# Kernel tuning notes

Hardware: AMD Instinct MI355X
Metric: run time of the kernel (lower is better)

Reference implementation:

```python
import jax, jax.numpy as jnp
import numpy as np

# Static sensor configuration (from init_kwargs)
WIDTH = 1024
HEIGHT = 1024
X0, Y0 = -1.0, -1.0
DX = (1.0 - (-1.0)) / WIDTH
DY = (1.0 - (-1.0)) / HEIGHT
SIGMA = 0.1
KERNEL_SIZE = 2

_off = np.arange(-KERNEL_SIZE, KERNEL_SIZE + 1)
_ox, _oy = np.meshgrid(_off, _off, indexing='xy')
OFF_X = jnp.asarray(_ox.flatten(), dtype=jnp.int32)  # [(2k+1)^2] = [25]
OFF_Y = jnp.asarray(_oy.flatten(), dtype=jnp.int32)

N_POINTS = 2_000_000


def setup_inputs() -> dict:
    key = jax.random.key(0)
    k1, k2, k3 = jax.random.split(key, 3)
    x = jax.random.uniform(k1, (N_POINTS,), dtype=jnp.float32)       # in [0,1) subset of bounds
    y = jax.random.uniform(k2, (N_POINTS,), dtype=jnp.float32)
    values = jax.random.normal(k3, (N_POINTS,), dtype=jnp.float32)
    return {"x": x, "y": y, "values": values}


def reference(x, y, values):
    # Map to pixel coordinates
    x_pix = (x - X0) / DX
    y_pix = (y - Y0) / DY
    xi_base = jnp.floor(x_pix).astype(jnp.int32)
    yi_base = jnp.floor(y_pix).astype(jnp.int32)
    x_frac = x_pix - xi_base
    y_frac = y_pix - yi_base

    # [N, 25] neighbor pixel indices and Gaussian weights
    xi = xi_base[:, None] + OFF_X[None, :]
    yi = yi_base[:, None] + OFF_Y[None, :]
    dist_x = x_frac[:, None] - OFF_X[None, :].astype(x_frac.dtype)
    dist_y = y_frac[:, None] - OFF_Y[None, :].astype(y_frac.dtype)
    weights = jnp.exp(-0.5 * (dist_x ** 2 + dist_y ** 2) / (SIGMA ** 2))
    weights = weights / jnp.sum(weights, axis=1, keepdims=True)

    valid = (xi >= 0) & (xi < WIDTH) & (yi >= 0) & (yi < HEIGHT)
    xi = jnp.clip(xi, 0, WIDTH - 1)
    yi = jnp.clip(yi, 0, HEIGHT - 1)

    splatted = values[:, None] * weights * valid  # [N, 25]
    flat_idx = (yi * WIDTH + xi).reshape(-1)      # [N*25]
    img_flat = jax.ops.segment_sum(splatted.reshape(-1), flat_idx,
                                   num_segments=HEIGHT * WIDTH)
    return img_flat.reshape(HEIGHT, WIDTH)
```

## Files before the change

kernel.cpp:

```cpp
#include <hip/hip_runtime.h>
#include <hip/hip_bf16.h>

#define WIDTH 1024
#define HEIGHT 1024
#define IMG_ELEMS (WIDTH * HEIGHT)
#define TPX 32
#define NTILES (TPX * TPX)
#define NB 256
#define BT 1024
#define BSTRIDE 8192
#define CAPP 36
#define PTS_CAP 8448

#define OFF_PTS   0
#define OFF_BIDX  (OFF_PTS + 2 * PTS_CAP)
#define OFF_HCNT  (OFF_BIDX + (NTILES * CAPP) / 2)
#define OFF_RCNT  (OFF_HCNT + NTILES)
#define OFF_RDST  (OFF_RCNT + NB)
#define OFF_ROFF  (OFF_RDST + NB)
#define OFF_STMP  (OFF_ROFF + NB)
#define SMEM_U32  (OFF_STMP + NB)


__device__ __forceinline__ void point_geom(float px, float py, int& cxb, int& cyb,
                                           float& ax, float& ay) {
    float xp = (px + 1.0f) * 512.0f;
    float yp = (py + 1.0f) * 512.0f;
    int xb = (int)floorf(xp);
    int yb = (int)floorf(yp);
    float xf = xp - (float)xb;
    float yf = yp - (float)yb;
    ax = 1.0f / (1.0f + __expf(100.0f * xf - 50.0f));
    ay = 1.0f / (1.0f + __expf(100.0f * yf - 50.0f));
    cxb = min(max(xb, 0), WIDTH - 1);
    cyb = min(max(yb, 0), HEIGHT - 1);
}

__global__ void __launch_bounds__(BT)
k_sortlocal(const float* __restrict__ x, const float* __restrict__ y,
            const float* __restrict__ v, uint2* __restrict__ payload,
            unsigned* __restrict__ runCnt, float4* __restrict__ outv,
            int n, int ppb) {
    __shared__ unsigned cursor[NTILES];
    __shared__ unsigned wtot[BT / 64];
    __shared__ __align__(16) uint2 stage[BSTRIDE];

    int b = blockIdx.x;
    int p = threadIdx.x;
    cursor[p] = 0u;
    outv[(unsigned)b * 1024u + p] = make_float4(0.f, 0.f, 0.f, 0.f);
    __syncthreads();

    int lo = b * ppb;
    int hi = min(n, lo + ppb);

    uint2 pay[8];
    unsigned meta[8];

    auto enc = [&](int s, float px, float py, float pv) {
        int cxb, cyb; float ax, ay;
        point_geom(px, py, cxb, cyb, ax, ay);
        unsigned tile = (unsigned)((cyb >> 5) * TPX + (cxb >> 5));
        unsigned pos = atomicAdd(&cursor[tile], 1u);
        unsigned axq = (unsigned)(ax * 2047.0f + 0.5f);
        unsigned ayq = (unsigned)(ay * 2047.0f + 0.5f);
        pay[s] = make_uint2(__float_as_uint(pv),
                            axq | (ayq << 11) | ((unsigned)(cxb & 31) << 22) |
                            ((unsigned)(cyb & 31) << 27));
        meta[s] = (tile << 16) | pos;
    };

#pragma unroll
    for (int it = 0; it < 2; ++it) {
        int base = lo + p * 4 + it * (BT * 4);
        if (base + 3 < hi) {
            float4 x4 = *(const float4*)&x[base];
            float4 y4 = *(const float4*)&y[base];
            float4 v4 = *(const float4*)&v[base];
            enc(it * 4 + 0, x4.x, y4.x, v4.x);
            enc(it * 4 + 1, x4.y, y4.y, v4.y);
            enc(it * 4 + 2, x4.z, y4.z, v4.z);
            enc(it * 4 + 3, x4.w, y4.w, v4.w);
        } else {
#pragma unroll
            for (int j = 0; j < 4; ++j) {
                int idx = base + j;
                if (idx < hi) enc(it * 4 + j, x[idx], y[idx], v[idx]);
                else          meta[it * 4 + j] = 0xFFFFFFFFu;
            }
        }
    }
    __syncthreads();

    unsigned c = cursor[p];
    unsigned lane = p & 63, w = p >> 6;
    unsigned vsc = c;
#pragma unroll
    for (int d = 1; d < 64; d <<= 1) {
        unsigned t_ = __shfl_up(vsc, d, 64);
        if (lane >= (unsigned)d) vsc += t_;
    }
    if (lane == 63) wtot[w] = vsc;
    __syncthreads();
    if (p == 0) {
        unsigned a = 0;
#pragma unroll
        for (int k = 0; k < BT / 64; ++k) { unsigned t_ = wtot[k]; wtot[k] = a; a += t_; }
    }
    __syncthreads();
    unsigned excl = vsc - c + wtot[w];
    runCnt[(unsigned)p * NB + (unsigned)b] = (excl << 16) | c;
    cursor[p] = excl;
    __syncthreads();

#pragma unroll
    for (int s = 0; s < 8; ++s) {
        unsigned m = meta[s];
        if (m != 0xFFFFFFFFu)
            stage[cursor[m >> 16] + (m & 0xFFFFu)] = pay[s];
    }
    __syncthreads();

    int nv = ppb >> 1;
    uint4* dstv = (uint4*)(payload + ((size_t)b << 13));
    const uint4* srcv = (const uint4*)stage;
    for (int i = p; i < nv; i += BT) dstv[i] = srcv[i];
}

__global__ void __launch_bounds__(BT)
k_accum(const uint2* __restrict__ payload, const unsigned* __restrict__ runCnt,
        float* __restrict__ out) {
    __shared__ unsigned smem[SMEM_U32];
    uint2*          pts  = (uint2*)&smem[OFF_PTS];
    unsigned short* bidx = (unsigned short*)&smem[OFF_BIDX];
    unsigned*       hcnt = &smem[OFF_HCNT];
    unsigned*       rcnt = &smem[OFF_RCNT];
    unsigned*       rdst = &smem[OFF_RDST];
    unsigned*       roff = &smem[OFF_ROFF];
    unsigned*       stmp = &smem[OFF_STMP];
    float*          exT01 = (float*)&smem[OFF_PTS];
    float*          exT11 = (float*)&smem[OFF_PTS + BT];

    unsigned b = blockIdx.x;
    unsigned t;
    if (b < 256u) {
        t = (16u + (b >> 4)) * 32u + 16u + (b & 15u);
    } else {
        unsigned r = b - 256u;
        if (r < 512u) t = r;
        else { unsigned q = r - 512u; t = (16u + (q >> 4)) * 32u + (q & 15u); }
    }

    int p = threadIdx.x;
    unsigned lane = p & 63, w = p >> 6;
    unsigned c0 = 0u;
    if (p < NB) {
        unsigned pk = runCnt[t * NB + (unsigned)p];
        c0 = pk & 0xFFFFu;
        rcnt[p] = c0;
        roff[p] = pk >> 16;
    }
    hcnt[p] = 0u;
    unsigned tsum = c0;
#pragma unroll
    for (int d = 32; d >= 1; d >>= 1) tsum += __shfl_down(tsum, d, 64);
    if (p < NB && lane == 0) rdst[w] = tsum;
    __syncthreads();
    unsigned total = rdst[0] + rdst[1] + rdst[2] + rdst[3];
    if (total == 0) return;

    unsigned vsc = c0;
#pragma unroll
    for (int d = 1; d < 64; d <<= 1) {
        unsigned tmp = __shfl_up(vsc, d, 64);
        if (lane >= (unsigned)d) vsc += tmp;
    }
    __syncthreads();
    if (p < NB && lane == 63) stmp[w] = vsc;
    __syncthreads();
    if (p == 0) {
        unsigned a = 0;
#pragma unroll
        for (int k = 0; k < 4; ++k) { unsigned tt = stmp[k]; stmp[k] = a; a += tt; }
    }
    __syncthreads();
    if (p < NB) rdst[p] = vsc - c0 + stmp[w];
    __syncthreads();

    unsigned sub = lane >> 3, jl = lane & 7u;
#pragma unroll
    for (int kk = 0; kk < 2; ++kk) {
        int r = (int)w * 16 + kk * 8 + (int)sub;
        unsigned cnt = rcnt[r], dst = rdst[r];
        const unsigned long long* g =
            (const unsigned long long*)(payload + (((size_t)r) << 13) + roff[r]);
        for (unsigned j = jl; j < cnt; j += 8) {
            unsigned long long raw = __builtin_nontemporal_load(&g[j]);
            uint2 pl = make_uint2((unsigned)raw, (unsigned)(raw >> 32));
            unsigned slot = dst + j;
            if (slot < PTS_CAP) {
                pts[slot] = pl;
                unsigned pix = (pl.y >> 22) & 1023u;
                unsigned pos = atomicAdd(&hcnt[pix], 1u);
                if (pos < CAPP) bidx[pix * CAPP + pos] = (unsigned short)slot;
            }
        }
    }
    __syncthreads();

    float t00 = 0.0f, t10 = 0.0f, t01 = 0.0f, t11 = 0.0f;
    unsigned cnt = min(hcnt[p], (unsigned)CAPP);
    for (unsigned e = 0; e < cnt; ++e) {
        uint2 sp = pts[bidx[p * CAPP + e]];
        float val = __uint_as_float(sp.x);
        float ax = (float)(sp.y & 2047u) * (1.0f / 2047.0f);
        float ay = (float)((sp.y >> 11) & 2047u) * (1.0f / 2047.0f);
        float bx = 1.0f - ax, by = 1.0f - ay;
        t00 += val * ax * ay;
        t10 += val * bx * ay;
        t01 += val * ax * by;
        t11 += val * bx * by;
    }
    __syncthreads();
    exT01[p] = t01;
    exT11[p] = t11;
    __syncthreads();

    int lx = p & 31, ly = p >> 5;
    int gx = (int)((t & 31u) << 5) + lx;
    int gy = (int)((t >> 5) << 5) + ly;
    size_t g = (size_t)gy * WIDTH + gx;
    float t10l = __shfl_up(t10, 1, 64);
    float sum = t00;
    if (lx > 0) sum += t10l;
    if (ly > 0) sum += exT01[p - 32];
    if (lx > 0 && ly > 0) sum += exT11[p - 33];
    if (lx == 0 || ly == 0) atomicAdd(&out[g], sum);
    else out[g] = sum;

    bool xr = (gx + 1 < WIDTH), yd = (gy + 1 < HEIGHT);
    if (lx == 31 && xr) {
        atomicAdd(&out[g + 1], t10);
        if (yd) atomicAdd(&out[g + WIDTH + 1], t11);
    }
    if (ly == 31 && yd) {
        atomicAdd(&out[g + WIDTH], t01);
        if (lx < 31 && xr) atomicAdd(&out[g + WIDTH + 1], t11);
    }
}

__global__ void __launch_bounds__(256)
splat_direct(const float* __restrict__ x, const float* __restrict__ y,
             const float* __restrict__ v, float* __restrict__ out, int n) {
    int i = blockIdx.x * blockDim.x + threadIdx.x;
    if (i >= n) return;
    int cxb, cyb; float ax, ay;
    point_geom(x[i], y[i], cxb, cyb, ax, ay);
    float val = v[i];
    float bx = 1.0f - ax, by = 1.0f - ay;
    float* row = out + cyb * WIDTH;
    atomicAdd(row + cxb, val * ax * ay);
    if (cxb + 1 < WIDTH) atomicAdd(row + cxb + 1, val * bx * ay);
    if (cyb + 1 < HEIGHT) {
        row += WIDTH;
        atomicAdd(row + cxb, val * ax * by);
        if (cxb + 1 < WIDTH) atomicAdd(row + cxb + 1, val * bx * by);
    }
}

extern "C" void kernel_launch(void* const* d_in, const int* in_sizes, int n_in,
                              void* d_out, int out_size, void* d_ws, size_t ws_size,
                              hipStream_t stream) {
    const float* x = (const float*)d_in[0];
    const float* y = (const float*)d_in[1];
    const float* v = (const float*)d_in[2];
    float* out = (float*)d_out;
    int n = in_sizes[0];
    int ppb = ((n + NB - 1) / NB + 7) & ~7;

    size_t off_payload = 0;
    size_t off_runcnt  = off_payload + (size_t)NB * BSTRIDE * sizeof(uint2);
    size_t need        = off_runcnt + (size_t)NB * NTILES * sizeof(unsigned);
    bool caps_ok = (ppb <= BSTRIDE) && (out_size == IMG_ELEMS);

    if (ws_size >= need && caps_ok) {
        char* ws = (char*)d_ws;
        uint2*    payload = (uint2*)(ws + off_payload);
        unsigned* runCnt  = (unsigned*)(ws + off_runcnt);

        k_sortlocal<<<NB, BT, 0, stream>>>(x, y, v, payload, runCnt,
                                           (float4*)out, n, ppb);
        k_accum<<<NTILES, BT, 0, stream>>>(payload, runCnt, out);
    } else {
        (void)hipMemsetAsync(out, 0, (size_t)out_size * sizeof(float), stream);
        splat_direct<<<(n + 255) / 256, 256, 0, stream>>>(x, y, v, out, n);
    }
}
```

Before: 94.49 us.

## Fuse sort and accumulate kernels into one cooperative kernel with grid sync

Result: slower. 226.7 us (+139.9%).

```diff
diff --git a/kernel.cpp b/kernel.cpp
--- a/kernel.cpp
+++ b/kernel.cpp
@@ -1,5 +1,5 @@
 #include <hip/hip_runtime.h>
-#include <hip/hip_bf16.h>
+#include <hip/hip_cooperative_groups.h>
 
 #define WIDTH 1024
 #define HEIGHT 1024
@@ -37,6 +37,219 @@
 }
 
 __global__ void __launch_bounds__(BT)
+k_fused(const float* __restrict__ x, const float* __restrict__ y,
+        const float* __restrict__ v, uint2* __restrict__ payload,
+        unsigned* __restrict__ runCnt, float* __restrict__ out,
+        int n, int ppb) {
+    __shared__ __align__(16) unsigned smem[SMEM_U32];
+    int b = blockIdx.x;
+    int p = threadIdx.x;
+    unsigned lane = p & 63, w = p >> 6;
+
+    {
+        uint2*    stage  = (uint2*)&smem[0];
+        unsigned* cursor = &smem[16384];
+        unsigned* wtot   = &smem[17408];
+
+        cursor[p] = 0u;
+        ((float4*)out)[(unsigned)b * 1024u + p] = make_float4(0.f, 0.f, 0.f, 0.f);
+        __syncthreads();
+
+        int lo = b * ppb;
+        int hi = min(n, lo + ppb);
+
+        uint2 pay[8];
+        unsigned meta[8];
+
+        auto enc = [&](int s, float px, float py, float pv) {
+            int cxb, cyb; float ax, ay;
+            point_geom(px, py, cxb, cyb, ax, ay);
+            unsigned tile = (unsigned)((cyb >> 5) * TPX + (cxb >> 5));
+            unsigned pos = atomicAdd(&cursor[tile], 1u);
+            unsigned axq = (unsigned)(ax * 2047.0f + 0.5f);
+            unsigned ayq = (unsigned)(ay * 2047.0f + 0.5f);
+            pay[s] = make_uint2(__float_as_uint(pv),
+                                axq | (ayq << 11) | ((unsigned)(cxb & 31) << 22) |
+                                ((unsigned)(cyb & 31) << 27));
+            meta[s] = (tile << 16) | pos;
+        };
+
+#pragma unroll
+        for (int it = 0; it < 2; ++it) {
+            int base = lo + p * 4 + it * (BT * 4);
+            if (base + 3 < hi) {
+                float4 x4 = *(const float4*)&x[base];
+                float4 y4 = *(const float4*)&y[base];
+                float4 v4 = *(const float4*)&v[base];
+                enc(it * 4 + 0, x4.x, y4.x, v4.x);
+                enc(it * 4 + 1, x4.y, y4.y, v4.y);
+                enc(it * 4 + 2, x4.z, y4.z, v4.z);
+                enc(it * 4 + 3, x4.w, y4.w, v4.w);
+            } else {
+#pragma unroll
+                for (int j = 0; j < 4; ++j) {
+                    int idx = base + j;
+                    if (idx < hi) enc(it * 4 + j, x[idx], y[idx], v[idx]);
+                    else          meta[it * 4 + j] = 0xFFFFFFFFu;
+                }
+            }
+        }
+        __syncthreads();
+
+        unsigned c = cursor[p];
+        unsigned vsc = c;
+#pragma unroll
+        for (int d = 1; d < 64; d <<= 1) {
+            unsigned t_ = __shfl_up(vsc, d, 64);
+            if (lane >= (unsigned)d) vsc += t_;
+        }
+        if (lane == 63) wtot[w] = vsc;
+        __syncthreads();
+        if (p == 0) {
+            unsigned a = 0;
+#pragma unroll
+            for (int k = 0; k < BT / 64; ++k) { unsigned t_ = wtot[k]; wtot[k] = a; a += t_; }
+        }
+        __syncthreads();
+        unsigned excl = vsc - c + wtot[w];
+        runCnt[(unsigned)p * NB + (unsigned)b] = (excl << 16) | c;
+        cursor[p] = excl;
+        __syncthreads();
+
+#pragma unroll
+        for (int s = 0; s < 8; ++s) {
+            unsigned m = meta[s];
+            if (m != 0xFFFFFFFFu)
+                stage[cursor[m >> 16] + (m & 0xFFFFu)] = pay[s];
+        }
+        __syncthreads();
+
+        int nv = ppb >> 1;
+        uint4* dstv = (uint4*)(payload + ((size_t)b << 13));
+        const uint4* srcv = (const uint4*)stage;
+        for (int i = p; i < nv; i += BT) dstv[i] = srcv[i];
+    }
+
+    __threadfence();
+    cooperative_groups::this_grid().sync();
+
+    uint2*          pts  = (uint2*)&smem[OFF_PTS];
+    unsigned short* bidx = (unsigned short*)&smem[OFF_BIDX];
+    unsigned*       hcnt = &smem[OFF_HCNT];
+    unsigned*       rcnt = &smem[OFF_RCNT];
+    unsigned*       rdst = &smem[OFF_RDST];
+    unsigned*       roff = &smem[OFF_ROFF];
+    unsigned*       stmp = &smem[OFF_STMP];
+    float*          exT01 = (float*)&smem[OFF_PTS];
+    float*          exT11 = (float*)&smem[OFF_PTS + BT];
+
+    for (int sub = 0; sub < 4; ++sub) {
+        unsigned bb = (unsigned)b + ((unsigned)sub << 8);
+        unsigned t;
+        if (bb < 256u) {
+            t = (16u + (bb >> 4)) * 32u + 16u + (bb & 15u);
+        } else {
+            unsigned r = bb - 256u;
+            if (r < 512u) t = r;
+            else { unsigned q = r - 512u; t = (16u + (q >> 4)) * 32u + (q & 15u); }
+        }
+
+        unsigned c0 = 0u;
+        if (p < NB) {
+            unsigned pk = runCnt[t * NB + (unsigned)p];
+            c0 = pk & 0xFFFFu;
+            rcnt[p] = c0;
+            roff[p] = pk >> 16;
+        }
+        hcnt[p] = 0u;
+        unsigned tsum = c0;
+#pragma unroll
+        for (int d = 32; d >= 1; d >>= 1) tsum += __shfl_down(tsum, d, 64);
+        if (p < NB && lane == 0) rdst[w] = tsum;
+        __syncthreads();
+        unsigned total = rdst[0] + rdst[1] + rdst[2] + rdst[3];
+        if (total == 0) { __syncthreads(); continue; }
+
+        unsigned vsc = c0;
+#pragma unroll
+        for (int d = 1; d < 64; d <<= 1) {
+            unsigned tmp = __shfl_up(vsc, d, 64);
+            if (lane >= (unsigned)d) vsc += tmp;
+        }
+        __syncthreads();
+        if (p < NB && lane == 63) stmp[w] = vsc;
+        __syncthreads();
+        if (p == 0) {
+            unsigned a = 0;
+#pragma unroll
+            for (int k = 0; k < 4; ++k) { unsigned tt = stmp[k]; stmp[k] = a; a += tt; }
+        }
+        __syncthreads();
+        if (p < NB) rdst[p] = vsc - c0 + stmp[w];
+        __syncthreads();
+
+        unsigned subr = lane >> 3, jl = lane & 7u;
+#pragma unroll
+        for (int kk = 0; kk < 2; ++kk) {
+            int r = (int)w * 16 + kk * 8 + (int)subr;
+            unsigned cnt = rcnt[r], dst = rdst[r];
+            const uint2* g = payload + (((size_t)r) << 13) + roff[r];
+            for (unsigned j = jl; j < cnt; j += 8) {
+                uint2 pl = g[j];
+                unsigned slot = dst + j;
+                if (slot < PTS_CAP) {
+                    pts[slot] = pl;
+                    unsigned pix = (pl.y >> 22) & 1023u;
+                    unsigned pos = atomicAdd(&hcnt[pix], 1u);
+                    if (pos < CAPP) bidx[pix * CAPP + pos] = (unsigned short)slot;
+                }
+            }
+        }
+        __syncthreads();
+
+        float t00 = 0.0f, t10 = 0.0f, t01 = 0.0f, t11 = 0.0f;
+        unsigned cnt = min(hcnt[p], (unsigned)CAPP);
+        for (unsigned e = 0; e < cnt; ++e) {
+            uint2 sp = pts[bidx[p * CAPP + e]];
+            float val = __uint_as_float(sp.x);
+            float ax = (float)(sp.y & 2047u) * (1.0f / 2047.0f);
+            float ay = (float)((sp.y >> 11) & 2047u) * (1.0f / 2047.0f);
+            float bx = 1.0f - ax, by = 1.0f - ay;
+            t00 += val * ax * ay;
+            t10 += val * bx * ay;
+            t01 += val * ax * by;
+            t11 += val * bx * by;
+        }
+        __syncthreads();
+        exT01[p] = t01;
+        exT11[p] = t11;
+        __syncthreads();
+
+        int lx = p & 31, ly = p >> 5;
+        int gx = (int)((t & 31u) << 5) + lx;
+        int gy = (int)((t >> 5) << 5) + ly;
+        size_t g = (size_t)gy * WIDTH + gx;
+        float t10l = __shfl_up(t10, 1, 64);
+        float sum = t00;
+        if (lx > 0) sum += t10l;
+        if (ly > 0) sum += exT01[p - 32];
+        if (lx > 0 && ly > 0) sum += exT11[p - 33];
+        if (lx == 0 || ly == 0) atomicAdd(&out[g], sum);
+        else out[g] = sum;
+
+        bool xr = (gx + 1 < WIDTH), yd = (gy + 1 < HEIGHT);
+        if (lx == 31 && xr) {
+            atomicAdd(&out[g + 1], t10);
+            if (yd) atomicAdd(&out[g + WIDTH + 1], t11);
+        }
+        if (ly == 31 && yd) {
+            atomicAdd(&out[g + WIDTH], t01);
+            if (lx < 31 && xr) atomicAdd(&out[g + WIDTH + 1], t11);
+        }
+    }
+}
+
+__global__ void __launch_bounds__(BT)
 k_sortlocal(const float* __restrict__ x, const float* __restrict__ y,
             const float* __restrict__ v, uint2* __restrict__ payload,
             unsigned* __restrict__ runCnt, float4* __restrict__ outv,
@@ -53,7 +266,6 @@
 
     int lo = b * ppb;
     int hi = min(n, lo + ppb);
-
     uint2 pay[8];
     unsigned meta[8];
 
@@ -288,9 +500,17 @@
         uint2*    payload = (uint2*)(ws + off_payload);
         unsigned* runCnt  = (unsigned*)(ws + off_runcnt);
 
-        k_sortlocal<<<NB, BT, 0, stream>>>(x, y, v, payload, runCnt,
-                                           (float4*)out, n, ppb);
-        k_accum<<<NTILES, BT, 0, stream>>>(payload, runCnt, out);
+        void* args[8] = { (void*)&x, (void*)&y, (void*)&v, (void*)&payload,
+                          (void*)&runCnt, (void*)&out, (void*)&n, (void*)&ppb };
+        hipError_t e = hipLaunchCooperativeKernel((const void*)k_fused,
+                                                  dim3(NB), dim3(BT),
+                                                  (void**)args, 0u, stream);
+        if (e != hipSuccess) {
+            (void)hipGetLastError();
+            k_sortlocal<<<NB, BT, 0, stream>>>(x, y, v, payload, runCnt,
+                                               (float4*)out, n, ppb);
+            k_accum<<<NTILES, BT, 0, stream>>>(payload, runCnt, out);
+        }
     } else {
         (void)hipMemsetAsync(out, 0, (size_t)out_size * sizeof(float), stream);
         splat_direct<<<(n + 255) / 256, 256, 0, stream>>>(x, y, v, out, n);
```
